# Kernel optimization log

Measured on AMD Instinct MI355X. Metric: run time of the kernel, lower is better.

Reference implementation:

```python
import jax, jax.numpy as jnp
import numpy as np

N_NODES = 100000


def gcn_conv(x, src, dst, norm, W, b):
    # PyG GCNConv: linear transform first, then normalized scatter-add aggregation, then bias.
    xw = x @ W                                   # [N, out]
    msgs = xw[src] * norm[:, None]               # [E+N, out] gathered, degree-normalized messages
    out = jax.ops.segment_sum(msgs, dst, num_segments=N_NODES)
    return out + b


def _build_graph(edge_index):
    # add self-loops (PyG gcn_norm default)
    loop = jnp.arange(N_NODES, dtype=edge_index.dtype)
    src = jnp.concatenate([edge_index[0], loop])
    dst = jnp.concatenate([edge_index[1], loop])
    deg = jax.ops.segment_sum(jnp.ones_like(dst, dtype=jnp.float32), dst, num_segments=N_NODES)
    dis = jnp.where(deg > 0, jax.lax.rsqrt(jnp.maximum(deg, 1.0)), 0.0)
    norm = dis[src] * dis[dst]                   # D^-1/2 (A+I) D^-1/2 edge weights
    return src, dst, norm


def setup_inputs() -> dict:
    key = jax.random.key(0)
    ks = jax.random.split(key, 6)
    F_IN, H, C, E = 128, 128, 8, 1600000
    x = jax.random.normal(ks[0], (N_NODES, F_IN), dtype=jnp.float32)
    edge_index = jax.random.randint(ks[1], (2, E), 0, N_NODES, dtype=jnp.int64)
    # glorot-style init for conv weights
    W1 = jax.random.normal(ks[2], (F_IN, H), dtype=jnp.float32) * (1.0 / np.sqrt(F_IN))
    b1 = jnp.zeros((H,), dtype=jnp.float32)
    W2 = jax.random.normal(ks[3], (H, C), dtype=jnp.float32) * (1.0 / np.sqrt(H))
    b2 = jnp.zeros((C,), dtype=jnp.float32)
    return {"x": x, "edge_index": edge_index, "W1": W1, "b1": b1, "W2": W2, "b2": b2}


def reference(x, edge_index, W1, b1, W2, b2):
    src, dst, norm = _build_graph(edge_index)
    h = gcn_conv(x, src, dst, norm, W1, b1)
    h = jax.nn.relu(h)
    # dropout is identity in eval mode
    out = gcn_conv(h, src, dst, norm, W2, b2)
    return jax.nn.log_softmax(out, axis=1)
```

## Files before the change

kernel.cpp:

```cpp
#include <hip/hip_runtime.h>

#define N_NODES 100000
#define NBKT 782
#define EPB 2048
#define SL_U 400000

typedef unsigned int uint;
typedef unsigned short ushort;
typedef __attribute__((ext_vector_type(8))) short bf16x8;
typedef __attribute__((ext_vector_type(4))) float f32x4;
typedef __attribute__((ext_vector_type(2))) float f32x2;

union FragU { uint4 u; bf16x8 b; };

__device__ __forceinline__ uint pack_bf16_2(float a, float b) {
    uint ua = __float_as_uint(a), ub = __float_as_uint(b);
    ua += 0x7fff + ((ua >> 16) & 1);
    ub += 0x7fff + ((ub >> 16) & 1);
    return (ua >> 16) | (ub & 0xffff0000u);
}

__device__ __forceinline__ int edge_at(const int* __restrict__ ei, int idx, int is64) {
    return is64 ? ei[2 * idx] : ei[idx];
}

__device__ __forceinline__ int block_probe_is64(const int* __restrict__ ei, int* sh) {
    int t = threadIdx.x;
    if (t == 0) *sh = 0;
    __syncthreads();
    int any = 0;
    for (int j = t; j < 4096; j += blockDim.x) any |= ei[2 * j + 1];
    if (any) atomicOr(sh, 1);
    __syncthreads();
    return (*sh == 0);
}

__global__ __launch_bounds__(256) void kA1(const int* __restrict__ ei, int E,
                                           int* __restrict__ slab,
                                           int* __restrict__ gflag) {
    __shared__ int h[NBKT];
    __shared__ int shp;
    int t = threadIdx.x;
    int is64 = block_probe_is64(ei, &shp);
    if (blockIdx.x == 0 && t == 0) gflag[0] = is64 ? 0 : 1;
    for (int i = t; i < NBKT; i += 256) h[i] = 0;
    __syncthreads();
    int base = blockIdx.x * EPB;
    int end = min(base + EPB, E);
    for (int e = base + t; e < end; e += 256) {
        int d = edge_at(ei, E + e, is64);
        atomicAdd(&h[d >> 7], 1);
    }
    __syncthreads();
    for (int i = t; i < NBKT; i += 256)
        slab[(size_t)blockIdx.x * NBKT + i] = h[i];
}

__global__ __launch_bounds__(256) void kA2a(int* __restrict__ slab, int PB,
                                            int* __restrict__ bkt_cnt) {
    int w = threadIdx.x >> 6;
    int l = threadIdx.x & 63;
    int k = blockIdx.x * 4 + w;
    if (k >= NBKT) return;
    int carry = 0;
    for (int base = 0; base < PB; base += 64) {
        int row = base + l;
        int v = (row < PB) ? slab[(size_t)row * NBKT + k] : 0;
        int incl = v;
#pragma unroll
        for (int d = 1; d < 64; d <<= 1) {
            int y = __shfl_up(incl, d, 64);
            if (l >= d) incl += y;
        }
        if (row < PB) slab[(size_t)row * NBKT + k] = carry + incl - v;
        carry += __shfl(incl, 63, 64);
    }
    if (l == 0) bkt_cnt[k] = carry;
}

__global__ __launch_bounds__(1024) void kA2b(const int* __restrict__ bkt_cnt,
                                             int* __restrict__ bkt_off) {
    __shared__ int s[1024];
    int t = threadIdx.x;
    int v = (t < NBKT) ? bkt_cnt[t] : 0;
    s[t] = v;
    __syncthreads();
    for (int d = 1; d < 1024; d <<= 1) {
        int y = (t >= d) ? s[t - d] : 0;
        __syncthreads();
        s[t] += y;
        __syncthreads();
    }
    if (t < NBKT) bkt_off[t] = s[t] - v;
}

__global__ __launch_bounds__(256) void kA3(const int* __restrict__ ei, int E,
                                           const int* __restrict__ gflag,
                                           const int* __restrict__ slab,
                                           const int* __restrict__ bkt_off,
                                           uint* __restrict__ bkt_data) {
    __shared__ int h[NBKT];
    __shared__ int pre[NBKT];
    int t = threadIdx.x;
    int is64 = (gflag[0] == 0);
    for (int i = t; i < NBKT; i += 256) {
        h[i] = 0;
        pre[i] = bkt_off[i] + slab[(size_t)blockIdx.x * NBKT + i];
    }
    __syncthreads();
    int lo = blockIdx.x * EPB;
    int end = min(lo + EPB, E);
    for (int e = lo + t; e < end; e += 256) {
        int d = edge_at(ei, E + e, is64);
        int s = edge_at(ei, e, is64);
        int b = d >> 7;
        int r = atomicAdd(&h[b], 1);
        bkt_data[pre[b] + r] = ((uint)s << 7) | (uint)(d & 127);
    }
}

__global__ __launch_bounds__(256) void kB(const uint* __restrict__ bkt_data,
                                          const int* __restrict__ bkt_off,
                                          const int* __restrict__ bkt_cnt,
                                          int* __restrict__ srcs,
                                          int* __restrict__ count,
                                          int* __restrict__ offs,
                                          float* __restrict__ dis,
                                          float* __restrict__ y2) {
    __shared__ int lc[128];
    __shared__ int sc[128];
    __shared__ int lcur[128];
    int t = threadIdx.x;
    int b = blockIdx.x;
    {
        int zb = b * 1024;
        int ze = min(zb + 1024, N_NODES * 8);
        for (int i = zb + t; i < ze; i += 256) y2[i] = 0.0f;
    }
    if (t < 128) { lc[t] = 0; lcur[t] = 0; }
    __syncthreads();
    int start = bkt_off[b];
    int n = bkt_cnt[b];
    for (int i = t; i < n; i += 256)
        atomicAdd(&lc[bkt_data[start + i] & 127], 1);
    __syncthreads();
    if (t < 128) sc[t] = lc[t];
    __syncthreads();
    for (int d = 1; d < 128; d <<= 1) {
        int y = 0;
        if (t < 128 && t >= d) y = sc[t - d];
        __syncthreads();
        if (t < 128) sc[t] += y;
        __syncthreads();
    }
    if (t < 128) {
        int node = b * 128 + t;
        if (node < N_NODES) {
            int c = lc[t];
            count[node] = c;
            offs[node] = start + sc[t] - c;
            dis[node] = rsqrtf((float)c + 1.0f);
        }
    }
    __syncthreads();
    for (int i = t; i < n; i += 256) {
        uint rec = bkt_data[start + i];
        int dl = rec & 127;
        int r = atomicAdd(&lcur[dl], 1);
        srcs[start + (sc[dl] - lc[dl]) + r] = rec >> 7;
    }
}

__global__ __launch_bounds__(256) void k_gemm1(const float* __restrict__ x,
                                               const float* __restrict__ W,
                                               const float* __restrict__ dis,
                                               uint* __restrict__ y1s) {
    __shared__ uint4 WtA[2048];
    char* wt = (char*)WtA;
    int t = threadIdx.x;

    const float4* W4 = (const float4*)W;
#pragma unroll
    for (int ii = 0; ii < 4; ++ii) {
        int tile = t + 256 * ii;
        int nq = tile >> 5, kq = tile & 31;
        float4 r0 = W4[(4 * kq + 0) * 32 + nq];
        float4 r1 = W4[(4 * kq + 1) * 32 + nq];
        float4 r2 = W4[(4 * kq + 2) * 32 + nq];
        float4 r3 = W4[(4 * kq + 3) * 32 + nq];
        const float* p0 = (const float*)&r0;
        const float* p1 = (const float*)&r1;
        const float* p2 = (const float*)&r2;
        const float* p3 = (const float*)&r3;
#pragma unroll
        for (int cc = 0; cc < 4; ++cc) {
            int n = 4 * nq + cc;
            uint2 v;
            v.x = pack_bf16_2(p0[cc], p1[cc]);
            v.y = pack_bf16_2(p2[cc], p3[cc]);
            *(uint2*)(wt + n * 256 + (((kq >> 1) ^ (n & 7)) << 4) + ((kq & 1) << 3)) = v;
        }
    }
    __syncthreads();

    int w = t >> 6, lane = t & 63;
    int m = lane & 15, kg = lane >> 4;
    int row0 = blockIdx.x * 64 + 16 * w;

    int arow = row0 + m;
    bool av = arow < N_NODES;
    const float4* xr = (const float4*)(x + (size_t)arow * 128);
    float4 z4 = make_float4(0.f, 0.f, 0.f, 0.f);
    FragU af[4];
#pragma unroll
    for (int kf = 0; kf < 4; ++kf) {
        float4 g0 = av ? xr[8 * kf + 2 * kg]     : z4;
        float4 g1 = av ? xr[8 * kf + 2 * kg + 1] : z4;
        const float* a0 = (const float*)&g0;
        const float* a1 = (const float*)&g1;
        af[kf].u.x = pack_bf16_2(a0[0], a0[1]);
        af[kf].u.y = pack_bf16_2(a0[2], a0[3]);
        af[kf].u.z = pack_bf16_2(a1[0], a1[1]);
        af[kf].u.w = pack_bf16_2(a1[2], a1[3]);
    }

    int crow = row0 + 4 * kg;
    float dd[4];
#pragma unroll
    for (int rr = 0; rr < 4; ++rr)
        dd[rr] = (crow + rr < N_NODES) ? dis[crow + rr] : 0.0f;

    char* yb = (char*)y1s;
#pragma unroll
    for (int ct = 0; ct < 8; ++ct) {
        f32x4 acc = {0.f, 0.f, 0.f, 0.f};
#pragma unroll
        for (int kf = 0; kf < 4; ++kf) {
            int n = 16 * ct + m;
            bf16x8 bw = *(const bf16x8*)(wt + n * 256 + ((((kf << 2) | kg) ^ (n & 7)) << 4));
            acc = __builtin_amdgcn_mfma_f32_16x16x32_bf16(af[kf].b, bw, acc, 0, 0, 0);
        }
#pragma unroll
        for (int rr = 0; rr < 4; ++rr) {
            float v = acc[rr] * dd[rr];
            float p = __shfl_xor(v, 1, 64);
            if (!(lane & 1)) {
                int grow = crow + rr;
                if (grow < N_NODES) {
                    uint pk = __builtin_amdgcn_cvt_pk_fp8_f32(v, p, 0, false);
                    *(ushort*)(yb + (size_t)ct * (SL_U * 4) + grow * 16 + m) = (ushort)pk;
                }
            }
        }
    }
}

__global__ __launch_bounds__(256) void k_agg1s(const uint* __restrict__ y1s,
                                               const int* __restrict__ srcs,
                                               const int* __restrict__ offs,
                                               const int* __restrict__ count,
                                               const float* __restrict__ dis,
                                               const float* __restrict__ b1,
                                               const float* __restrict__ W2,
                                               float* __restrict__ y2) {
    int t = threadIdx.x;
    int slice = blockIdx.x & 7;
    int nb = blockIdx.x >> 3;
    int g = t >> 3;
    int j = t & 7;
    int d = nb * 32 + g;

    float w0[8], w1[8];
    const float* wr0 = W2 + (size_t)(slice * 16 + 2 * j) * 8;
#pragma unroll
    for (int c = 0; c < 8; ++c) { w0[c] = wr0[c]; w1[c] = wr0[8 + c]; }

    const uint4* ybase = (const uint4*)(y1s + (size_t)slice * SL_U);
    f32x2 acc2[8];
#pragma unroll
    for (int c = 0; c < 8; ++c) acc2[c] = (f32x2){0.f, 0.f};

#define ACCUM_Q(q)                                                             \
    do {                                                                       \
        acc2[0] += __builtin_amdgcn_cvt_pk_f32_fp8((q).x, false);              \
        acc2[1] += __builtin_amdgcn_cvt_pk_f32_fp8((q).x, true);               \
        acc2[2] += __builtin_amdgcn_cvt_pk_f32_fp8((q).y, false);              \
        acc2[3] += __builtin_amdgcn_cvt_pk_f32_fp8((q).y, true);               \
        acc2[4] += __builtin_amdgcn_cvt_pk_f32_fp8((q).z, false);              \
        acc2[5] += __builtin_amdgcn_cvt_pk_f32_fp8((q).z, true);               \
        acc2[6] += __builtin_amdgcn_cvt_pk_f32_fp8((q).w, false);              \
        acc2[7] += __builtin_amdgcn_cvt_pk_f32_fp8((q).w, true);               \
    } while (0)

    int st = offs[d], n = count[d];
    int i = j;
    if (i <= n) {
        int sk = (i < n) ? srcs[st + i] : d;
        uint4 q = ybase[sk];
        for (i += 8; i <= n; i += 8) {
            int sk2 = (i < n) ? srcs[st + i] : d;
            uint4 qn = ybase[sk2];
            ACCUM_Q(q);
            q = qn;
        }
        ACCUM_Q(q);
    }
#undef ACCUM_Q

    float acc[16];
#pragma unroll
    for (int c = 0; c < 8; ++c) { acc[2 * c] = acc2[c][0]; acc[2 * c + 1] = acc2[c][1]; }

    int hi4 = (j >> 2) & 1, hi2 = (j >> 1) & 1, hi1 = j & 1;
    float v8[8];
#pragma unroll
    for (int c = 0; c < 8; ++c) {
        float keep = hi4 ? acc[c + 8] : acc[c];
        float send = hi4 ? acc[c] : acc[c + 8];
        v8[c] = keep + __shfl_xor(send, 4, 8);
    }
    float v4[4];
#pragma unroll
    for (int c = 0; c < 4; ++c) {
        float keep = hi2 ? v8[c + 4] : v8[c];
        float send = hi2 ? v8[c] : v8[c + 4];
        v4[c] = keep + __shfl_xor(send, 2, 8);
    }
    float v2[2];
#pragma unroll
    for (int c = 0; c < 2; ++c) {
        float keep = hi1 ? v4[c + 2] : v4[c];
        float send = hi1 ? v4[c] : v4[c + 2];
        v2[c] = keep + __shfl_xor(send, 1, 8);
    }

    float ddv = dis[d];
    float2 b = ((const float2*)b1)[slice * 8 + j];
    float h0 = fmaxf(fmaf(v2[0], ddv, b.x), 0.0f);
    float h1 = fmaxf(fmaf(v2[1], ddv, b.y), 0.0f);

    float p[8];
#pragma unroll
    for (int c = 0; c < 8; ++c) p[c] = h0 * w0[c] + h1 * w1[c];
    float q4[4];
#pragma unroll
    for (int c = 0; c < 4; ++c) {
        float keep = hi4 ? p[c + 4] : p[c];
        float send = hi4 ? p[c] : p[c + 4];
        q4[c] = keep + __shfl_xor(send, 4, 8);
    }
    float q2[2];
#pragma unroll
    for (int c = 0; c < 2; ++c) {
        float keep = hi2 ? q4[c + 2] : q4[c];
        float send = hi2 ? q4[c] : q4[c + 2];
        q2[c] = keep + __shfl_xor(send, 2, 8);
    }
    float keep = hi1 ? q2[1] : q2[0];
    float send = hi1 ? q2[0] : q2[1];
    float q = keep + __shfl_xor(send, 1, 8);

    atomicAdd(&y2[(size_t)d * 8 + j], q * ddv);
}

__global__ __launch_bounds__(256) void k_agg2(const float* __restrict__ y2,
                                              const int* __restrict__ srcs,
                                              const int* __restrict__ offs,
                                              const int* __restrict__ count,
                                              const float* __restrict__ dis,
                                              const float* __restrict__ b2,
                                              float* __restrict__ out) {
    int t = threadIdx.x;
    int g = (blockIdx.x * 256 + t) >> 3;
    int j = t & 7;
    if (g >= N_NODES) return;
    const float4* yb = (const float4*)y2;
    float acc[8];
#pragma unroll
    for (int c = 0; c < 8; ++c) acc[c] = 0.0f;
    int st = offs[g], n = count[g];
    for (int i = j; i <= n; i += 8) {
        int sk = g;
        if (i < n) sk = srcs[st + i];
        float4 a = yb[(size_t)sk * 2];
        float4 b = yb[(size_t)sk * 2 + 1];
        acc[0] += a.x; acc[1] += a.y; acc[2] += a.z; acc[3] += a.w;
        acc[4] += b.x; acc[5] += b.y; acc[6] += b.z; acc[7] += b.w;
    }
    int hi4 = (j >> 2) & 1, hi2 = (j >> 1) & 1, hi1 = j & 1;
    float v4[4];
#pragma unroll
    for (int c = 0; c < 4; ++c) {
        float keep = hi4 ? acc[c + 4] : acc[c];
        float send = hi4 ? acc[c] : acc[c + 4];
        v4[c] = keep + __shfl_xor(send, 4, 8);
    }
    float v2[2];
#pragma unroll
    for (int c = 0; c < 2; ++c) {
        float keep = hi2 ? v4[c + 2] : v4[c];
        float send = hi2 ? v4[c] : v4[c + 2];
        v2[c] = keep + __shfl_xor(send, 2, 8);
    }
    float keep = hi1 ? v2[1] : v2[0];
    float send = hi1 ? v2[0] : v2[1];
    float q = keep + __shfl_xor(send, 1, 8);

    float o = fmaf(q, dis[g], b2[j]);
    float m = o;
#pragma unroll
    for (int k = 1; k < 8; k <<= 1) m = fmaxf(m, __shfl_xor(m, k, 64));
    float e = expf(o - m);
    float ssum = e;
#pragma unroll
    for (int k = 1; k < 8; k <<= 1) ssum += __shfl_xor(ssum, k, 64);
    out[(size_t)g * 8 + j] = (o - m) - logf(ssum);
}

extern "C" void kernel_launch(void* const* d_in, const int* in_sizes, int n_in,
                              void* d_out, int out_size, void* d_ws, size_t ws_size,
                              hipStream_t stream) {
    const float* x  = (const float*)d_in[0];
    const int*   ei = (const int*)d_in[1];
    const float* W1 = (const float*)d_in[2];
    const float* b1 = (const float*)d_in[3];
    const float* W2 = (const float*)d_in[4];
    const float* b2 = (const float*)d_in[5];
    float* out = (float*)d_out;
    const int E = in_sizes[1] / 2;
    const int PB = (E + EPB - 1) / EPB;
    const int Epad = (E + 3) & ~3;
    int slabInts = (PB * NBKT + 3) & ~3;

    int*   slab     = (int*)d_ws;
    int*   bkt_cnt  = slab + slabInts;
    int*   bkt_off  = bkt_cnt + 784;
    int*   gflag    = bkt_off + 784;
    int*   count    = gflag + 4;
    int*   offs     = count + N_NODES;
    float* dis      = (float*)(offs + N_NODES);
    uint*  bkt_data = (uint*)(dis + N_NODES);
    int*   srcs     = (int*)(bkt_data + Epad);
    uint*  y1s      = (uint*)(srcs + Epad);
    float* y2       = (float*)(y1s + (size_t)8 * SL_U);

    kA1    <<<PB, 256, 0, stream>>>(ei, E, slab, gflag);
    kA2a   <<<(NBKT + 3) / 4, 256, 0, stream>>>(slab, PB, bkt_cnt);
    kA2b   <<<1, 1024, 0, stream>>>(bkt_cnt, bkt_off);
    kA3    <<<PB, 256, 0, stream>>>(ei, E, gflag, slab, bkt_off, bkt_data);
    kB     <<<NBKT, 256, 0, stream>>>(bkt_data, bkt_off, bkt_cnt, srcs, count, offs, dis, y2);

    k_gemm1<<<(N_NODES + 63) / 64, 256, 0, stream>>>(x, W1, dis, y1s);
    k_agg1s<<<8 * 3125, 256, 0, stream>>>(y1s, srcs, offs, count, dis, b1, W2, y2);
    k_agg2 <<<(N_NODES * 8 + 255) / 256, 256, 0, stream>>>(y2, srcs, offs, count, dis, b2, out);
}
```

Before: 203.2 us.

## Pack layer-2 features to bf16 before gather aggregation; enlarge edge partition block

Adds a pack kernel that converts the fp32 layer-2 node features (8 per node) to bf16, so each gathered neighbor row in k_agg2 is one 16-byte load instead of two. The aggregation unpacks to fp32 and accumulates with packed float2 adds. It also raises edges-per-block in the bucketing phase from 2048 to 8192, cutting the partition block count and the slab size. The cost is an extra kernel launch and bf16 rounding of the second-layer messages before the log_softmax, which lowers accuracy.

```diff
diff --git a/kernel.cpp b/kernel.cpp
--- a/kernel.cpp
+++ b/kernel.cpp
@@ -2,7 +2,7 @@
 
 #define N_NODES 100000
 #define NBKT 782
-#define EPB 2048
+#define EPB 8192
 #define SL_U 400000
 
 typedef unsigned int uint;
@@ -19,6 +19,8 @@
     ub += 0x7fff + ((ub >> 16) & 1);
     return (ua >> 16) | (ub & 0xffff0000u);
 }
+__device__ __forceinline__ float bf_lo(uint u) { return __uint_as_float(u << 16); }
+__device__ __forceinline__ float bf_hi(uint u) { return __uint_as_float(u & 0xffff0000u); }
 
 __device__ __forceinline__ int edge_at(const int* __restrict__ ei, int idx, int is64) {
     return is64 ? ei[2 * idx] : ei[idx];
@@ -363,7 +365,20 @@
     atomicAdd(&y2[(size_t)d * 8 + j], q * ddv);
 }
 
-__global__ __launch_bounds__(256) void k_agg2(const float* __restrict__ y2,
+__global__ __launch_bounds__(256) void k_pack(const float4* __restrict__ y2q,
+                                              uint4* __restrict__ y2b) {
+    int i = blockIdx.x * 256 + threadIdx.x;
+    if (i >= N_NODES) return;
+    float4 a = y2q[2 * i], b = y2q[2 * i + 1];
+    uint4 o;
+    o.x = pack_bf16_2(a.x, a.y);
+    o.y = pack_bf16_2(a.z, a.w);
+    o.z = pack_bf16_2(b.x, b.y);
+    o.w = pack_bf16_2(b.z, b.w);
+    y2b[i] = o;
+}
+
+__global__ __launch_bounds__(256) void k_agg2(const uint4* __restrict__ y2b,
                                               const int* __restrict__ srcs,
                                               const int* __restrict__ offs,
                                               const int* __restrict__ count,
@@ -374,19 +389,23 @@
     int g = (blockIdx.x * 256 + t) >> 3;
     int j = t & 7;
     if (g >= N_NODES) return;
-    const float4* yb = (const float4*)y2;
-    float acc[8];
-#pragma unroll
-    for (int c = 0; c < 8; ++c) acc[c] = 0.0f;
+    f32x2 acc2[4];
+#pragma unroll
+    for (int c = 0; c < 4; ++c) acc2[c] = (f32x2){0.f, 0.f};
     int st = offs[g], n = count[g];
     for (int i = j; i <= n; i += 8) {
         int sk = g;
         if (i < n) sk = srcs[st + i];
-        float4 a = yb[(size_t)sk * 2];
-        float4 b = yb[(size_t)sk * 2 + 1];
-        acc[0] += a.x; acc[1] += a.y; acc[2] += a.z; acc[3] += a.w;
-        acc[4] += b.x; acc[5] += b.y; acc[6] += b.z; acc[7] += b.w;
-    }
+        uint4 q = y2b[sk];
+        acc2[0] += (f32x2){bf_lo(q.x), bf_hi(q.x)};
+        acc2[1] += (f32x2){bf_lo(q.y), bf_hi(q.y)};
+        acc2[2] += (f32x2){bf_lo(q.z), bf_hi(q.z)};
+        acc2[3] += (f32x2){bf_lo(q.w), bf_hi(q.w)};
+    }
+    float acc[8];
+#pragma unroll
+    for (int c = 0; c < 4; ++c) { acc[2 * c] = acc2[c][0]; acc[2 * c + 1] = acc2[c][1]; }
+
     int hi4 = (j >> 2) & 1, hi2 = (j >> 1) & 1, hi1 = j & 1;
     float v4[4];
 #pragma unroll
@@ -443,6 +462,7 @@
     int*   srcs     = (int*)(bkt_data + Epad);
     uint*  y1s      = (uint*)(srcs + Epad);
     float* y2       = (float*)(y1s + (size_t)8 * SL_U);
+    uint4* y2b      = (uint4*)(y2 + (size_t)N_NODES * 8);
 
     kA1    <<<PB, 256, 0, stream>>>(ei, E, slab, gflag);
     kA2a   <<<(NBKT + 3) / 4, 256, 0, stream>>>(slab, PB, bkt_cnt);
@@ -452,5 +472,6 @@
 
     k_gemm1<<<(N_NODES + 63) / 64, 256, 0, stream>>>(x, W1, dis, y1s);
     k_agg1s<<<8 * 3125, 256, 0, stream>>>(y1s, srcs, offs, count, dis, b1, W2, y2);
-    k_agg2 <<<(N_NODES * 8 + 255) / 256, 256, 0, stream>>>(y2, srcs, offs, count, dis, b2, out);
-}
+    k_pack <<<(N_NODES + 255) / 256, 256, 0, stream>>>((const float4*)y2, y2b);
+    k_agg2 <<<(N_NODES * 8 + 255) / 256, 256, 0, stream>>>(y2b, srcs, offs, count, dis, b2, out);
+}
```

Result: faster. 195.9 us (-3.6%).
